# Performance work log

Measured on AMD Instinct MI355X. Metric: run time of the kernel, lower is better.

## Reference

```python
import jax, jax.numpy as jnp
import numpy as np

# model dims (match init_kwargs)
EMBED_DIM = 1024
NUM_HEADS = 16
HEAD_DIM = EMBED_DIM // NUM_HEADS  # 64
WS = 256           # window_size[0]*window_size[1] = 16*16
NW = 64            # number of windows
M = NW * WS        # gathered length = 16384
L = M - 1          # raw tokens (padding row appended makes M rows)
SCALE = HEAD_DIM ** -0.5


def _rope(t, cos, sin):
    # t: [M, H, d]; cos/sin: [M, d] -> broadcast over heads
    c = cos[:, None, :]
    s = sin[:, None, :]
    half = HEAD_DIM // 2
    rot = jnp.concatenate([-t[..., half:], t[..., :half]], axis=-1)
    return t * c + rot * s


def setup_inputs() -> dict:
    key = jax.random.key(0)
    ks = jax.random.split(key, 8)
    x = jax.random.normal(ks[0], (L, EMBED_DIM), jnp.float32)
    # kv_indices: permutation of all M rows (incl. padding row index L) so every
    # token lands in exactly one window slot, as the scatter-back assumes.
    kv_indices = jax.random.permutation(ks[1], M).astype(jnp.int64)
    q_indices = kv_indices            # unused in the manual (non-xformers) branch
    inv_indices = jnp.arange(L, dtype=jnp.int64)  # unused in the manual branch
    # rotary tables over gathered positions
    pos = jnp.arange(M, dtype=jnp.float32)
    inv_freq = 1.0 / (10000.0 ** (jnp.arange(0, HEAD_DIM, 2, dtype=jnp.float32) / HEAD_DIM))
    ang = pos[:, None] * inv_freq[None, :]          # [M, d/2]
    ang = jnp.concatenate([ang, ang], axis=-1)      # [M, d]
    rope_cos = jnp.cos(ang)
    rope_sin = jnp.sin(ang)
    # learned params
    qkv_w = jax.random.normal(ks[2], (3 * EMBED_DIM, EMBED_DIM), jnp.float32) * (EMBED_DIM ** -0.5)
    qkv_b = jax.random.normal(ks[3], (3 * EMBED_DIM,), jnp.float32) * 0.02
    proj_w = jax.random.normal(ks[4], (EMBED_DIM, EMBED_DIM), jnp.float32) * (EMBED_DIM ** -0.5)
    proj_b = jax.random.normal(ks[5], (EMBED_DIM,), jnp.float32) * 0.02
    padding = jnp.zeros((1, EMBED_DIM), jnp.float32)  # nn.Parameter(torch.zeros(1, D))
    return {"x": x, "qkv_w": qkv_w, "qkv_b": qkv_b, "proj_w": proj_w,
            "proj_b": proj_b, "padding": padding, "rope_cos": rope_cos,
            "rope_sin": rope_sin, "kv_indices": kv_indices,
            "q_indices": q_indices, "inv_indices": inv_indices, "ws": WS}


def reference(x, qkv_w, qkv_b, proj_w, proj_b, padding, rope_cos, rope_sin,
              kv_indices, q_indices, inv_indices, ws):
    # append padding row: [L+1, D]
    xp = jnp.concatenate([x, padding], axis=0)
    # fused qkv projection -> [M, 3, H, d]
    qkv = (xp @ qkv_w.T + qkv_b).reshape(-1, 3, NUM_HEADS, HEAD_DIM)
    q, k, v = qkv[:, 0], qkv[:, 1], qkv[:, 2]
    # manual windowed branch: gather q/k/v with kv_indices, RoPE (mode='key') on q and k
    qg = _rope(q[kv_indices], rope_cos, rope_sin)   # [M, H, d]
    kg = _rope(k[kv_indices], rope_cos, rope_sin)
    vg = v[kv_indices]
    nw = M // ws
    qw = qg.reshape(nw, ws, NUM_HEADS, HEAD_DIM)
    kw = kg.reshape(nw, ws, NUM_HEADS, HEAD_DIM)
    vw = vg.reshape(nw, ws, NUM_HEADS, HEAD_DIM)
    attn = jax.nn.softmax(SCALE * jnp.einsum('wind,wjnd->wnij', qw, kw), axis=-1)
    ow = jnp.einsum('wnij,wjnd->wind', attn, vw).reshape(M, NUM_HEADS * HEAD_DIM)
    # scatter back to original token order, drop padding row
    ori = jnp.zeros((M, EMBED_DIM), x.dtype).at[kv_indices].set(ow)
    out = ori[:L] @ proj_w.T + proj_b
    return out
```

## Files before the change

### kernel.cpp

```cpp
#include <hip/hip_runtime.h>
#include <hip/hip_bf16.h>

#define EMBED 1024
#define THREE_EMBED 3072
#define NHEAD 16
#define HDIM 64
#define MTOT 16384
#define LTOT 16383

typedef __attribute__((ext_vector_type(8))) short bf16x8;
typedef __attribute__((ext_vector_type(4))) float f32x4;

__device__ __forceinline__ unsigned short f2b(float f) {
  union { float f; unsigned u; } v; v.f = f;
  unsigned r = v.u + 0x7fffu + ((v.u >> 16) & 1u);
  return (unsigned short)(r >> 16);
}
__device__ __forceinline__ float b2f(unsigned short h) {
  union { unsigned u; float f; } v; v.u = ((unsigned)h) << 16;
  return v.f;
}

__device__ __forceinline__ void gload16(const void* g, void* l) {
  __builtin_amdgcn_global_load_lds(
      (const __attribute__((address_space(1))) void*)g,
      (__attribute__((address_space(3))) void*)l, 16, 0, 0);
}

#define BARRIER() asm volatile("s_barrier" ::: "memory")

__global__ __launch_bounds__(256) void cast_inputs(
    const float* __restrict__ x, const float* __restrict__ padding,
    const float* __restrict__ wq, const int* __restrict__ kvi,
    unsigned short* __restrict__ xb, unsigned short* __restrict__ wqb,
    int* __restrict__ inv)
{
  const int NX = MTOT * EMBED / 8;
  const int NQ = THREE_EMBED * EMBED / 8;
  const int total = NX + NQ;
  int g = blockIdx.x * 256 + threadIdx.x;
  const int stride = gridDim.x * 256;
  for (; g < total + MTOT; g += stride) {
    if (g >= total) {
      int i = g - total;
      inv[kvi[i]] = i;
      continue;
    }
    const float* src;
    unsigned short* dst;
    if (g < NX) {
      size_t e = (size_t)g * 8;
      int row = (int)(e >> 10);
      src = (row < LTOT) ? (x + e) : (padding + (e - (size_t)LTOT * 1024));
      dst = xb + e;
    } else {
      size_t e = (size_t)(g - NX) * 8;
      src = wq + e;
      dst = wqb + e;
    }
    float4 a = *(const float4*)src;
    float4 b = *(const float4*)(src + 4);
    ushort4 u0, u1;
    u0.x = f2b(a.x); u0.y = f2b(a.y); u0.z = f2b(a.z); u0.w = f2b(a.w);
    u1.x = f2b(b.x); u1.y = f2b(b.y); u1.z = f2b(b.z); u1.w = f2b(b.w);
    *(ushort4*)dst = u0;
    *(ushort4*)(dst + 4) = u1;
  }
}

template <int EPI>
__global__ __launch_bounds__(512, 2) void gemm256(
    const unsigned short* __restrict__ A, const unsigned short* __restrict__ B,
    const float* __restrict__ bias, const int* __restrict__ inv,
    unsigned short* __restrict__ outb, float* __restrict__ outf)
{
  __shared__ __align__(16) unsigned short lds[65536];
  const int t = threadIdx.x;
  const int lane = t & 63, wid = t >> 6;
  const int l15 = lane & 15, quad = lane >> 4;
  const int wr = wid >> 2, wc = wid & 3;
  const int bm = blockIdx.x, bn = blockIdx.y;

  const int srow = wid * 8 + (lane >> 3);
  const int scol = ((lane & 7) ^ (lane >> 3)) * 8;
  const unsigned short* gA = A + (size_t)(bm * 256 + srow) * EMBED + scol;
  const unsigned short* gB = B + (size_t)(bn * 256 + srow) * EMBED + scol;

  auto stA = [&](int p, int R0, int kt) {
    const unsigned short* g = gA + (size_t)R0 * EMBED + kt * 64;
    char* d = (char*)lds + p * 32768 + R0 * 128 + wid * 1024;
    gload16(g, d);
    gload16(g + (size_t)64 * EMBED, d + 8192);
  };
  auto stB = [&](int p, int R0, int kt) {
    const unsigned short* g = gB + (size_t)R0 * EMBED + kt * 64;
    char* d = (char*)lds + 65536 + p * 32768 + R0 * 128 + wid * 1024;
    gload16(g, d);
    gload16(g + (size_t)64 * EMBED, d + 8192);
  };

  const int aOff = (wr * 128 + l15) * 64;
  const int bOff = (wc * 64 + l15) * 64;
  const int swz0 = (quad ^ (l15 & 7)) * 8;
  const int swz1 = ((quad + 4) ^ (l15 & 7)) * 8;

  f32x4 acc[8][4];
#pragma unroll
  for (int i = 0; i < 8; ++i)
#pragma unroll
    for (int j = 0; j < 4; ++j) acc[i][j] = (f32x4){0.f, 0.f, 0.f, 0.f};

  stA(0, 0, 0); stA(0, 128, 0); stB(0, 0, 0); stB(0, 128, 0);
  stB(1, 0, 1); stB(1, 128, 1);
  asm volatile("s_waitcnt vmcnt(4)" ::: "memory");
  BARRIER();

#define MFMA16(m0, m1)                                                       \
  do {                                                                       \
    _Pragma("unroll") for (int nt = 0; nt < 4; ++nt)                         \
        acc[m0][nt] = __builtin_amdgcn_mfma_f32_16x16x32_bf16(               \
            a00, b0[nt], acc[m0][nt], 0, 0, 0);                              \
    _Pragma("unroll") for (int nt = 0; nt < 4; ++nt)                         \
        acc[m1][nt] = __builtin_amdgcn_mfma_f32_16x16x32_bf16(               \
            a10, b0[nt], acc[m1][nt], 0, 0, 0);                              \
    _Pragma("unroll") for (int nt = 0; nt < 4; ++nt)                         \
        acc[m0][nt] = __builtin_amdgcn_mfma_f32_16x16x32_bf16(               \
            a01, b1[nt], acc[m0][nt], 0, 0, 0);                              \
    _Pragma("unroll") for (int nt = 0; nt < 4; ++nt)                         \
        acc[m1][nt] = __builtin_amdgcn_mfma_f32_16x16x32_bf16(               \
            a11, b1[nt], acc[m1][nt], 0, 0, 0);                              \
  } while (0)

  bf16x8 b0[4], b1[4];
#pragma unroll 1
  for (int tt = 0; tt < 16; ++tt) {
    const int p = tt & 1;
    const unsigned short* Ab = lds + p * 16384 + aOff;
    const unsigned short* Bb = lds + 32768 + p * 16384 + bOff;

    {
#pragma unroll
      for (int nt = 0; nt < 4; ++nt) {
        b0[nt] = *(const bf16x8*)(Bb + nt * 1024 + swz0);
        b1[nt] = *(const bf16x8*)(Bb + nt * 1024 + swz1);
      }
      bf16x8 a00 = *(const bf16x8*)(Ab + 0 * 1024 + swz0);
      bf16x8 a01 = *(const bf16x8*)(Ab + 0 * 1024 + swz1);
      bf16x8 a10 = *(const bf16x8*)(Ab + 1 * 1024 + swz0);
      bf16x8 a11 = *(const bf16x8*)(Ab + 1 * 1024 + swz1);
      if (tt < 15) stA(p ^ 1, 0, tt + 1);
      BARRIER();
      __builtin_amdgcn_s_setprio(1);
      MFMA16(0, 1);
      __builtin_amdgcn_s_setprio(0);
      BARRIER();
    }
    {
      bf16x8 a00 = *(const bf16x8*)(Ab + 2 * 1024 + swz0);
      bf16x8 a01 = *(const bf16x8*)(Ab + 2 * 1024 + swz1);
      bf16x8 a10 = *(const bf16x8*)(Ab + 3 * 1024 + swz0);
      bf16x8 a11 = *(const bf16x8*)(Ab + 3 * 1024 + swz1);
      if (tt < 15) stA(p ^ 1, 128, tt + 1);
      BARRIER();
      __builtin_amdgcn_s_setprio(1);
      MFMA16(2, 3);
      __builtin_amdgcn_s_setprio(0);
      BARRIER();
    }
    {
      bf16x8 a00 = *(const bf16x8*)(Ab + 4 * 1024 + swz0);
      bf16x8 a01 = *(const bf16x8*)(Ab + 4 * 1024 + swz1);
      bf16x8 a10 = *(const bf16x8*)(Ab + 5 * 1024 + swz0);
      bf16x8 a11 = *(const bf16x8*)(Ab + 5 * 1024 + swz1);
      if (tt < 14) stB(p, 0, tt + 2);
      BARRIER();
      __builtin_amdgcn_s_setprio(1);
      MFMA16(4, 5);
      __builtin_amdgcn_s_setprio(0);
      BARRIER();
    }
    {
      bf16x8 a00 = *(const bf16x8*)(Ab + 6 * 1024 + swz0);
      bf16x8 a01 = *(const bf16x8*)(Ab + 6 * 1024 + swz1);
      bf16x8 a10 = *(const bf16x8*)(Ab + 7 * 1024 + swz0);
      bf16x8 a11 = *(const bf16x8*)(Ab + 7 * 1024 + swz1);
      if (tt < 14) stB(p, 128, tt + 2);
      BARRIER();
      __builtin_amdgcn_s_setprio(1);
      MFMA16(6, 7);
      __builtin_amdgcn_s_setprio(0);
      if (tt < 14) {
        asm volatile("s_waitcnt vmcnt(4)" ::: "memory");
      } else if (tt == 14) {
        asm volatile("s_waitcnt vmcnt(0)" ::: "memory");
      }
      BARRIER();
    }
  }
#undef MFMA16

  float bv[4];
#pragma unroll
  for (int nt = 0; nt < 4; ++nt)
    bv[nt] = bias[bn * 256 + wc * 64 + nt * 16 + l15];
  if constexpr (EPI == 0) {
    const int hh = bn * 4 + wc;
    unsigned short* buf = outb + (size_t)hh * (MTOT * HDIM);
#pragma unroll
    for (int mt = 0; mt < 8; ++mt) {
#pragma unroll
      for (int reg = 0; reg < 4; ++reg) {
        int row = bm * 256 + wr * 128 + mt * 16 + quad * 4 + reg;
        int i = inv[row];
#pragma unroll
        for (int nt = 0; nt < 4; ++nt)
          buf[(size_t)i * HDIM + nt * 16 + l15] =
              f2b(acc[mt][nt][reg] + bv[nt]);
      }
    }
  } else {
    const int col = bn * 256 + wc * 64;
#pragma unroll
    for (int mt = 0; mt < 8; ++mt) {
#pragma unroll
      for (int reg = 0; reg < 4; ++reg) {
        int row = bm * 256 + wr * 128 + mt * 16 + quad * 4 + reg;
        if (row < LTOT) {
#pragma unroll
          for (int nt = 0; nt < 4; ++nt)
            outf[(size_t)row * EMBED + col + nt * 16 + l15] =
                acc[mt][nt][reg] + bv[nt];
        }
      }
    }
  }
}

__global__ __launch_bounds__(256) void rope_qk(
    const float* __restrict__ rope_cos, const float* __restrict__ rope_sin,
    unsigned short* __restrict__ qkvh)
{
  int g = blockIdx.x * 256 + threadIdx.x;
  int dc = g & 3;
  int i  = (g >> 2) & (MTOT - 1);
  int hh = g >> 16;
  unsigned short* p = qkvh + ((size_t)hh * MTOT + i) * HDIM;
  bf16x8 lo = *(const bf16x8*)(p + dc * 8);
  bf16x8 hi = *(const bf16x8*)(p + 32 + dc * 8);
  const float* cp = rope_cos + (size_t)i * HDIM + dc * 8;
  const float* sp = rope_sin + (size_t)i * HDIM + dc * 8;
  float cl[8], ch[8], sl[8], sh[8];
  *(float4*)(cl)     = *(const float4*)(cp);
  *(float4*)(cl + 4) = *(const float4*)(cp + 4);
  *(float4*)(ch)     = *(const float4*)(cp + 32);
  *(float4*)(ch + 4) = *(const float4*)(cp + 36);
  *(float4*)(sl)     = *(const float4*)(sp);
  *(float4*)(sl + 4) = *(const float4*)(sp + 4);
  *(float4*)(sh)     = *(const float4*)(sp + 32);
  *(float4*)(sh + 4) = *(const float4*)(sp + 36);
  const float sc = (hh < 16) ? 0.125f : 1.0f;
  bf16x8 olo, ohi;
#pragma unroll
  for (int j = 0; j < 8; ++j) {
    float a = b2f((unsigned short)lo[j]);
    float b = b2f((unsigned short)hi[j]);
    olo[j] = (short)f2b((a * cl[j] - b * sl[j]) * sc);
    ohi[j] = (short)f2b((b * ch[j] + a * sh[j]) * sc);
  }
  *(bf16x8*)(p + dc * 8) = olo;
  *(bf16x8*)(p + 32 + dc * 8) = ohi;
}

__global__ __launch_bounds__(256) void cast_w(
    const float* __restrict__ w, unsigned short* __restrict__ wb)
{
  int g = blockIdx.x * 256 + threadIdx.x;
  size_t e = (size_t)g * 8;
  float4 a = *(const float4*)(w + e);
  float4 b = *(const float4*)(w + e + 4);
  ushort4 u0, u1;
  u0.x = f2b(a.x); u0.y = f2b(a.y); u0.z = f2b(a.z); u0.w = f2b(a.w);
  u1.x = f2b(b.x); u1.y = f2b(b.y); u1.z = f2b(b.z); u1.w = f2b(b.w);
  *(ushort4*)(wb + e) = u0;
  *(ushort4*)(wb + e + 4) = u1;
}

__global__ __launch_bounds__(256, 4) void attn(
    const unsigned short* __restrict__ qkvh,
    const int* __restrict__ kvi,
    unsigned short* __restrict__ ori)
{
  __shared__ __align__(16) unsigned short sK[128 * 64];
  __shared__ __align__(16) unsigned short sV[64 * 128];
  __shared__ __align__(16) unsigned short sP[4][16 * 40];

  const int t = threadIdx.x;
  const int lane = t & 63, wid = t >> 6;
  const int l15 = lane & 15, quad = lane >> 4;
  const int wwin = blockIdx.x >> 4;
  const int h = blockIdx.x & 15;

  const unsigned short* Qh = qkvh + (size_t)h * (MTOT * HDIM);
  const unsigned short* Kh = qkvh + (size_t)(16 + h) * (MTOT * HDIM);
  const unsigned short* Vh = qkvh + (size_t)(32 + h) * (MTOT * HDIM);

  f32x4 accO[4][4];
  float mrow[4][4], lrow[4][4];
#pragma unroll
  for (int qt = 0; qt < 4; ++qt) {
#pragma unroll
    for (int nt = 0; nt < 4; ++nt) accO[qt][nt] = (f32x4){0.f, 0.f, 0.f, 0.f};
#pragma unroll
    for (int reg = 0; reg < 4; ++reg) { mrow[qt][reg] = -1e30f; lrow[qt][reg] = 0.f; }
  }

  bf16x8 qa[4][2];
#pragma unroll
  for (int qt = 0; qt < 4; ++qt) {
    int i = wwin * 256 + wid * 64 + qt * 16 + l15;
    const unsigned short* qp = Qh + (size_t)i * HDIM;
    qa[qt][0] = *(const bf16x8*)(qp + quad * 8);
    qa[qt][1] = *(const bf16x8*)(qp + 32 + quad * 8);
  }

  for (int half = 0; half < 2; ++half) {
    __syncthreads();
    {
      int key = t >> 1, hx = t & 1;
      int i = wwin * 256 + half * 128 + key;
      const unsigned short* kp = Kh + (size_t)i * HDIM + hx * 32;
#pragma unroll
      for (int cc = 0; cc < 4; ++cc) {
        int c = hx * 4 + cc;
        uint4 kv = *(const uint4*)(kp + cc * 8);
        *(uint4*)(sK + key * 64 + ((c ^ (key & 7)) * 8)) = kv;
      }
      const unsigned short* vp = Vh + (size_t)i * HDIM + hx * 32;
      int kc3 = key >> 3, k7 = key & 7;
#pragma unroll
      for (int c = 0; c < 4; ++c) {
        bf16x8 va = *(const bf16x8*)(vp + c * 8);
#pragma unroll
        for (int j = 0; j < 8; ++j) {
          int d = hx * 32 + c * 8 + j;
          sV[d * 128 + ((kc3 ^ (d & 7)) * 8) + k7] = (unsigned short)va[j];
        }
      }
    }
    __syncthreads();

#pragma unroll
    for (int qt = 0; qt < 4; ++qt) {
      f32x4 accS[8];
#pragma unroll
      for (int nt = 0; nt < 8; ++nt) accS[nt] = (f32x4){0.f, 0.f, 0.f, 0.f};
#pragma unroll
      for (int ks = 0; ks < 2; ++ks) {
#pragma unroll
        for (int nt = 0; nt < 8; ++nt) {
          int key = nt * 16 + l15;
          bf16x8 bk = *(const bf16x8*)(
              sK + key * 64 + (((ks * 4 + quad) ^ (key & 7)) * 8));
          accS[nt] = __builtin_amdgcn_mfma_f32_16x16x32_bf16(
              qa[qt][ks], bk, accS[nt], 0, 0, 0);
        }
      }
#pragma unroll
      for (int reg = 0; reg < 4; ++reg) {
        float mx = accS[0][reg];
#pragma unroll
        for (int nt = 1; nt < 8; ++nt) mx = fmaxf(mx, accS[nt][reg]);
#pragma unroll
        for (int off = 1; off < 16; off <<= 1)
          mx = fmaxf(mx, __shfl_xor(mx, off, 64));
        float mold = mrow[qt][reg];
        float mnew = fmaxf(mold, mx);
        float alpha = __expf(mold - mnew);
        mrow[qt][reg] = mnew;
        float ls = 0.f;
#pragma unroll
        for (int nt = 0; nt < 8; ++nt) {
          float p = __expf(accS[nt][reg] - mnew);
          accS[nt][reg] = p;
          ls += p;
        }
#pragma unroll
        for (int off = 1; off < 16; off <<= 1) ls += __shfl_xor(ls, off, 64);
        lrow[qt][reg] = lrow[qt][reg] * alpha + ls;
#pragma unroll
        for (int nt = 0; nt < 4; ++nt) accO[qt][nt][reg] *= alpha;
      }
#pragma unroll
      for (int kc = 0; kc < 4; ++kc) {
#pragma unroll
        for (int nt2 = 0; nt2 < 2; ++nt2) {
#pragma unroll
          for (int reg = 0; reg < 4; ++reg) {
            sP[wid][(quad * 4 + reg) * 40 + nt2 * 16 + l15] =
                f2b(accS[kc * 2 + nt2][reg]);
          }
        }
        bf16x8 pa = *(const bf16x8*)(&sP[wid][l15 * 40 + quad * 8]);
#pragma unroll
        for (int nt = 0; nt < 4; ++nt) {
          int d = nt * 16 + l15;
          bf16x8 bv = *(const bf16x8*)(
              sV + d * 128 + (((kc * 4 + quad) ^ (d & 7)) * 8));
          accO[qt][nt] = __builtin_amdgcn_mfma_f32_16x16x32_bf16(
              pa, bv, accO[qt][nt], 0, 0, 0);
        }
      }
    }
  }

#pragma unroll
  for (int qt = 0; qt < 4; ++qt) {
#pragma unroll
    for (int reg = 0; reg < 4; ++reg) {
      int i = wwin * 256 + wid * 64 + qt * 16 + quad * 4 + reg;
      int orow = kvi[i];
      float inv = 1.0f / lrow[qt][reg];
      unsigned short* op = ori + (size_t)orow * EMBED + h * HDIM;
#pragma unroll
      for (int nt = 0; nt < 4; ++nt) {
        op[nt * 16 + l15] = f2b(accO[qt][nt][reg] * inv);
      }
    }
  }
}

extern "C" void kernel_launch(void* const* d_in, const int* in_sizes, int n_in,
                              void* d_out, int out_size, void* d_ws, size_t ws_size,
                              hipStream_t stream) {
  const float* x        = (const float*)d_in[0];
  const float* qkv_w    = (const float*)d_in[1];
  const float* qkv_b    = (const float*)d_in[2];
  const float* proj_w   = (const float*)d_in[3];
  const float* proj_b   = (const float*)d_in[4];
  const float* padding  = (const float*)d_in[5];
  const float* rope_cos = (const float*)d_in[6];
  const float* rope_sin = (const float*)d_in[7];
  const int*   kvi      = (const int*)d_in[8];

  unsigned short* qkvh = (unsigned short*)d_ws;
  unsigned short* R    = (unsigned short*)((char*)d_ws +
                            (size_t)MTOT * THREE_EMBED * 2);
  unsigned short* xb  = R;
  unsigned short* ori = R;
  unsigned short* wqb = (unsigned short*)d_out;
  unsigned short* wpb = qkvh;
  int* inv = (int*)((char*)d_out + (size_t)LTOT * EMBED * 4 - (size_t)MTOT * 4);
  float* out = (float*)d_out;

  cast_inputs<<<4096, 256, 0, stream>>>(x, padding, qkv_w, kvi, xb, wqb, inv);
  gemm256<0><<<dim3(64, 12), 512, 0, stream>>>(xb, wqb, qkv_b, inv, qkvh,
                                               nullptr);
  rope_qk<<<8192, 256, 0, stream>>>(rope_cos, rope_sin, qkvh);
  attn<<<dim3(64 * 16), 256, 0, stream>>>(qkvh, kvi, ori);
  cast_w<<<512, 256, 0, stream>>>(proj_w, wpb);
  gemm256<1><<<dim3(64, 4), 512, 0, stream>>>(ori, wpb, proj_b, nullptr,
                                              nullptr, out);
}
```

Measured before the change: 416.4 us.

## Move scatter-back into projection GEMM epilogue and unroll K-loop by two

The attention kernel now writes its output contiguously in window order, and the projection GEMM scatters each output row to its original token position through kv_indices in the epilogue. The goal is to replace scattered bf16 stores in attention with contiguous ones and to move the scatter onto fp32 output rows. The GEMM main loop is also unrolled by two with compile-time ping-pong buffer indices and a peeled tail, which removes the per-iteration stage conditionals. The cost is scattered fp32 row writes in the projection epilogue and a larger unrolled code body.

```diff
diff --git a/kernel.cpp b/kernel.cpp
--- a/kernel.cpp
+++ b/kernel.cpp
@@ -71,7 +71,7 @@
 template <int EPI>
 __global__ __launch_bounds__(512, 2) void gemm256(
     const unsigned short* __restrict__ A, const unsigned short* __restrict__ B,
-    const float* __restrict__ bias, const int* __restrict__ inv,
+    const float* __restrict__ bias, const int* __restrict__ idx,
     unsigned short* __restrict__ outb, float* __restrict__ outf)
 {
   __shared__ __align__(16) unsigned short lds[65536];
@@ -131,72 +131,76 @@
             a11, b1[nt], acc[m1][nt], 0, 0, 0);                              \
   } while (0)
 
-  bf16x8 b0[4], b1[4];
+#define TILE(P, KT, STA, STB, WCNT)                                          \
+  {                                                                          \
+    const unsigned short* Ab = lds + (P) * 16384 + aOff;                     \
+    const unsigned short* Bb = lds + 32768 + (P) * 16384 + bOff;             \
+    bf16x8 b0[4], b1[4];                                                     \
+    {                                                           \
+      _Pragma("unroll") for (int nt = 0; nt < 4; ++nt) {                     \
+        b0[nt] = *(const bf16x8*)(Bb + nt * 1024 + swz0);                    \
+        b1[nt] = *(const bf16x8*)(Bb + nt * 1024 + swz1);                    \
+      }                                                                      \
+      bf16x8 a00 = *(const bf16x8*)(Ab + 0 * 1024 + swz0);                   \
+      bf16x8 a01 = *(const bf16x8*)(Ab + 0 * 1024 + swz1);                   \
+      bf16x8 a10 = *(const bf16x8*)(Ab + 1 * 1024 + swz0);                   \
+      bf16x8 a11 = *(const bf16x8*)(Ab + 1 * 1024 + swz1);                   \
+      if (STA) stA((P) ^ 1, 0, (KT) + 1);                                    \
+      BARRIER();                                                             \
+      __builtin_amdgcn_s_setprio(1);                                         \
+      MFMA16(0, 1);                                                          \
+      __builtin_amdgcn_s_setprio(0);                                         \
+      BARRIER();                                                             \
+    }                                                                        \
+    {                                                           \
+      bf16x8 a00 = *(const bf16x8*)(Ab + 2 * 1024 + swz0);                   \
+      bf16x8 a01 = *(const bf16x8*)(Ab + 2 * 1024 + swz1);                   \
+      bf16x8 a10 = *(const bf16x8*)(Ab + 3 * 1024 + swz0);                   \
+      bf16x8 a11 = *(const bf16x8*)(Ab + 3 * 1024 + swz1);                   \
+      if (STA) stA((P) ^ 1, 128, (KT) + 1);                                  \
+      BARRIER();                                                             \
+      __builtin_amdgcn_s_setprio(1);                                         \
+      MFMA16(2, 3);                                                          \
+      __builtin_amdgcn_s_setprio(0);                                         \
+      BARRIER();                                                             \
+    }                                                                        \
+    {                                                           \
+      bf16x8 a00 = *(const bf16x8*)(Ab + 4 * 1024 + swz0);                   \
+      bf16x8 a01 = *(const bf16x8*)(Ab + 4 * 1024 + swz1);                   \
+      bf16x8 a10 = *(const bf16x8*)(Ab + 5 * 1024 + swz0);                   \
+      bf16x8 a11 = *(const bf16x8*)(Ab + 5 * 1024 + swz1);                   \
+      if (STB) stB((P), 0, (KT) + 2);                                        \
+      BARRIER();                                                             \
+      __builtin_amdgcn_s_setprio(1);                                         \
+      MFMA16(4, 5);                                                          \
+      __builtin_amdgcn_s_setprio(0);                                         \
+      BARRIER();                                                             \
+    }                                                                        \
+    {                                                           \
+      bf16x8 a00 = *(const bf16x8*)(Ab + 6 * 1024 + swz0);                   \
+      bf16x8 a01 = *(const bf16x8*)(Ab + 6 * 1024 + swz1);                   \
+      bf16x8 a10 = *(const bf16x8*)(Ab + 7 * 1024 + swz0);                   \
+      bf16x8 a11 = *(const bf16x8*)(Ab + 7 * 1024 + swz1);                   \
+      if (STB) stB((P), 128, (KT) + 2);                                      \
+      BARRIER();                                                             \
+      __builtin_amdgcn_s_setprio(1);                                         \
+      MFMA16(6, 7);                                                          \
+      __builtin_amdgcn_s_setprio(0);                                         \
+      if ((WCNT) == 4) asm volatile("s_waitcnt vmcnt(4)" ::: "memory");      \
+      if ((WCNT) == 0) asm volatile("s_waitcnt vmcnt(0)" ::: "memory");      \
+      BARRIER();                                                             \
+    }                                                                        \
+  }
+
 #pragma unroll 1
-  for (int tt = 0; tt < 16; ++tt) {
-    const int p = tt & 1;
-    const unsigned short* Ab = lds + p * 16384 + aOff;
-    const unsigned short* Bb = lds + 32768 + p * 16384 + bOff;
-
-    {
-#pragma unroll
-      for (int nt = 0; nt < 4; ++nt) {
-        b0[nt] = *(const bf16x8*)(Bb + nt * 1024 + swz0);
-        b1[nt] = *(const bf16x8*)(Bb + nt * 1024 + swz1);
-      }
-      bf16x8 a00 = *(const bf16x8*)(Ab + 0 * 1024 + swz0);
-      bf16x8 a01 = *(const bf16x8*)(Ab + 0 * 1024 + swz1);
-      bf16x8 a10 = *(const bf16x8*)(Ab + 1 * 1024 + swz0);
-      bf16x8 a11 = *(const bf16x8*)(Ab + 1 * 1024 + swz1);
-      if (tt < 15) stA(p ^ 1, 0, tt + 1);
-      BARRIER();
-      __builtin_amdgcn_s_setprio(1);
-      MFMA16(0, 1);
-      __builtin_amdgcn_s_setprio(0);
-      BARRIER();
-    }
-    {
-      bf16x8 a00 = *(const bf16x8*)(Ab + 2 * 1024 + swz0);
-      bf16x8 a01 = *(const bf16x8*)(Ab + 2 * 1024 + swz1);
-      bf16x8 a10 = *(const bf16x8*)(Ab + 3 * 1024 + swz0);
-      bf16x8 a11 = *(const bf16x8*)(Ab + 3 * 1024 + swz1);
-      if (tt < 15) stA(p ^ 1, 128, tt + 1);
-      BARRIER();
-      __builtin_amdgcn_s_setprio(1);
-      MFMA16(2, 3);
-      __builtin_amdgcn_s_setprio(0);
-      BARRIER();
-    }
-    {
-      bf16x8 a00 = *(const bf16x8*)(Ab + 4 * 1024 + swz0);
-      bf16x8 a01 = *(const bf16x8*)(Ab + 4 * 1024 + swz1);
-      bf16x8 a10 = *(const bf16x8*)(Ab + 5 * 1024 + swz0);
-      bf16x8 a11 = *(const bf16x8*)(Ab + 5 * 1024 + swz1);
-      if (tt < 14) stB(p, 0, tt + 2);
-      BARRIER();
-      __builtin_amdgcn_s_setprio(1);
-      MFMA16(4, 5);
-      __builtin_amdgcn_s_setprio(0);
-      BARRIER();
-    }
-    {
-      bf16x8 a00 = *(const bf16x8*)(Ab + 6 * 1024 + swz0);
-      bf16x8 a01 = *(const bf16x8*)(Ab + 6 * 1024 + swz1);
-      bf16x8 a10 = *(const bf16x8*)(Ab + 7 * 1024 + swz0);
-      bf16x8 a11 = *(const bf16x8*)(Ab + 7 * 1024 + swz1);
-      if (tt < 14) stB(p, 128, tt + 2);
-      BARRIER();
-      __builtin_amdgcn_s_setprio(1);
-      MFMA16(6, 7);
-      __builtin_amdgcn_s_setprio(0);
-      if (tt < 14) {
-        asm volatile("s_waitcnt vmcnt(4)" ::: "memory");
-      } else if (tt == 14) {
-        asm volatile("s_waitcnt vmcnt(0)" ::: "memory");
-      }
-      BARRIER();
-    }
-  }
+  for (int t2 = 0; t2 < 7; ++t2) {
+    const int kt = t2 * 2;
+    TILE(0, kt, 1, 1, 4);
+    TILE(1, kt + 1, 1, 1, 4);
+  }
+  TILE(0, 14, 1, 0, 0);
+  TILE(1, 15, 0, 0, -1);
+#undef TILE
 #undef MFMA16
 
   float bv[4];
@@ -211,7 +215,7 @@
 #pragma unroll
       for (int reg = 0; reg < 4; ++reg) {
         int row = bm * 256 + wr * 128 + mt * 16 + quad * 4 + reg;
-        int i = inv[row];
+        int i = idx[row];
 #pragma unroll
         for (int nt = 0; nt < 4; ++nt)
           buf[(size_t)i * HDIM + nt * 16 + l15] =
@@ -224,11 +228,12 @@
     for (int mt = 0; mt < 8; ++mt) {
 #pragma unroll
       for (int reg = 0; reg < 4; ++reg) {
-        int row = bm * 256 + wr * 128 + mt * 16 + quad * 4 + reg;
-        if (row < LTOT) {
+        int i = bm * 256 + wr * 128 + mt * 16 + quad * 4 + reg;
+        int orow = idx[i];
+        if (orow < LTOT) {
 #pragma unroll
           for (int nt = 0; nt < 4; ++nt)
-            outf[(size_t)row * EMBED + col + nt * 16 + l15] =
+            outf[(size_t)orow * EMBED + col + nt * 16 + l15] =
                 acc[mt][nt][reg] + bv[nt];
         }
       }
@@ -287,8 +292,7 @@
 
 __global__ __launch_bounds__(256, 4) void attn(
     const unsigned short* __restrict__ qkvh,
-    const int* __restrict__ kvi,
-    unsigned short* __restrict__ ori)
+    unsigned short* __restrict__ ow)
 {
   __shared__ __align__(16) unsigned short sK[128 * 64];
   __shared__ __align__(16) unsigned short sV[64 * 128];
@@ -418,9 +422,8 @@
 #pragma unroll
     for (int reg = 0; reg < 4; ++reg) {
       int i = wwin * 256 + wid * 64 + qt * 16 + quad * 4 + reg;
-      int orow = kvi[i];
       float inv = 1.0f / lrow[qt][reg];
-      unsigned short* op = ori + (size_t)orow * EMBED + h * HDIM;
+      unsigned short* op = ow + (size_t)i * EMBED + h * HDIM;
 #pragma unroll
       for (int nt = 0; nt < 4; ++nt) {
         op[nt * 16 + l15] = f2b(accO[qt][nt][reg] * inv);
@@ -445,8 +448,8 @@
   unsigned short* qkvh = (unsigned short*)d_ws;
   unsigned short* R    = (unsigned short*)((char*)d_ws +
                             (size_t)MTOT * THREE_EMBED * 2);
-  unsigned short* xb  = R;
-  unsigned short* ori = R;
+  unsigned short* xb = R;
+  unsigned short* ow = R;
   unsigned short* wqb = (unsigned short*)d_out;
   unsigned short* wpb = qkvh;
   int* inv = (int*)((char*)d_out + (size_t)LTOT * EMBED * 4 - (size_t)MTOT * 4);
@@ -456,8 +459,8 @@
   gemm256<0><<<dim3(64, 12), 512, 0, stream>>>(xb, wqb, qkv_b, inv, qkvh,
                                                nullptr);
   rope_qk<<<8192, 256, 0, stream>>>(rope_cos, rope_sin, qkvh);
-  attn<<<dim3(64 * 16), 256, 0, stream>>>(qkvh, kvi, ori);
+  attn<<<dim3(64 * 16), 256, 0, stream>>>(qkvh, ow);
   cast_w<<<512, 256, 0, stream>>>(proj_w, wpb);
-  gemm256<1><<<dim3(64, 4), 512, 0, stream>>>(ori, wpb, proj_b, nullptr,
-                                              nullptr, out);
-}
+  gemm256<1><<<dim3(64, 4), 512, 0, stream>>>(ow, wpb, proj_b, kvi, nullptr,
+                                              out);
+}
```

After: 420.4 us. Within noise of the previous version (+1.0%).
